# Kernel tuning notes

Hardware: AMD Instinct MI355X
Metric: run time of the kernel (lower is better)

The kernel has to match this reference:

```python
import jax, jax.numpy as jnp
import numpy as np

EMBED_DIM = 1024
K_DIM = 64
NUM_HEADS = 16


def setup_inputs() -> dict:
    key = jax.random.key(0)
    kx, kq, kk, kv, kw = jax.random.split(key, 5)
    x = jax.random.normal(kx, (4, 2048, EMBED_DIM), dtype=jnp.float32)
    # per-head weights stacked along a leading head axis (torch.randn init)
    wq = jax.random.normal(kq, (NUM_HEADS, EMBED_DIM, K_DIM), dtype=jnp.float32)
    wk = jax.random.normal(kk, (NUM_HEADS, EMBED_DIM, K_DIM), dtype=jnp.float32)
    wv = jax.random.normal(kv, (NUM_HEADS, EMBED_DIM, K_DIM), dtype=jnp.float32)
    w = jax.random.normal(kw, (NUM_HEADS * K_DIM, EMBED_DIM), dtype=jnp.float32)
    return {"x": x, "wq": wq, "wk": wk, "wv": wv, "w": w}


def reference(x, wq, wk, wv, w):
    # x: [B,S,D]; wq/wk/wv: [H,D,K]; w: [H*K, D]
    q = jnp.einsum('bsd,hdk->bhsk', x, wq)
    k = jnp.einsum('bsd,hdk->bhsk', x, wk)
    v = jnp.einsum('bsd,hdk->bhsk', x, wv)
    scale = 1.0 / jnp.sqrt(jnp.asarray(K_DIM, x.dtype))
    scores = jnp.einsum('bhsk,bhtk->bhst', q, k) * scale  # [B,H,S,S]
    attn = jax.nn.softmax(scores, axis=-1)
    ctx = jnp.einsum('bhst,bhtk->bhsk', attn, v)  # [B,H,S,K]
    B, H, S, K = ctx.shape
    # concat heads along last dim in head order (matches torch.cat of per-head outs)
    heads = jnp.transpose(ctx, (0, 2, 1, 3)).reshape(B, S, H * K)
    return jnp.matmul(heads, w)  # [B,S,D]
```

## Files before the change

kernel.cpp:

```cpp
#include <hip/hip_runtime.h>
#include <hip/hip_bf16.h>
#include <math.h>

#define EMBED 1024
#define KD 64
#define NH 16
#define SEQ 2048
#define BATCH 4
#define BH (BATCH * NH)
#define NTOK ((size_t)BH * SEQ * KD)

typedef float4 f4;
typedef unsigned short u16;
typedef __attribute__((ext_vector_type(8))) short v8s;
typedef __attribute__((ext_vector_type(4))) float v4f;

__device__ __forceinline__ u16 f2bf(float f) {
    unsigned u = __float_as_uint(f);
    unsigned r = (u + 0x7fffu + ((u >> 16) & 1u)) >> 16;
    return (u16)r;
}
__device__ __forceinline__ float bf2f(u16 h) {
    return __uint_as_float(((unsigned)h) << 16);
}

__device__ __forceinline__ void gload_lds16(const void* g, void* l) {
    __builtin_amdgcn_global_load_lds(
        (const __attribute__((address_space(1))) unsigned int*)g,
        (__attribute__((address_space(3))) unsigned int*)l, 16, 0, 0);
}

__device__ __forceinline__ float dpp_max16(float v) {
    float t;
    t = __uint_as_float(__builtin_amdgcn_update_dpp(0, __float_as_uint(v), 0xB1, 0xF, 0xF, true));
    v = fmaxf(v, t);
    t = __uint_as_float(__builtin_amdgcn_update_dpp(0, __float_as_uint(v), 0x4E, 0xF, 0xF, true));
    v = fmaxf(v, t);
    t = __uint_as_float(__builtin_amdgcn_update_dpp(0, __float_as_uint(v), 0x124, 0xF, 0xF, true));
    v = fmaxf(v, t);
    t = __uint_as_float(__builtin_amdgcn_update_dpp(0, __float_as_uint(v), 0x128, 0xF, 0xF, true));
    v = fmaxf(v, t);
    return v;
}

__global__ __launch_bounds__(256)
void convert_x_kernel(const float* __restrict__ x,
                      u16* __restrict__ xh, u16* __restrict__ xl)
{
    size_t i = ((size_t)blockIdx.x * 256 + threadIdx.x) * 4;
    f4 v = *(const f4*)(x + i);
    u16 h0 = f2bf(v.x), h1 = f2bf(v.y), h2 = f2bf(v.z), h3 = f2bf(v.w);
    u16 l0 = f2bf(v.x - bf2f(h0)), l1 = f2bf(v.y - bf2f(h1));
    u16 l2 = f2bf(v.z - bf2f(h2)), l3 = f2bf(v.w - bf2f(h3));
    uint2 H, L;
    H.x = (unsigned)h0 | ((unsigned)h1 << 16);
    H.y = (unsigned)h2 | ((unsigned)h3 << 16);
    L.x = (unsigned)l0 | ((unsigned)l1 << 16);
    L.y = (unsigned)l2 | ((unsigned)l3 << 16);
    *(uint2*)(xh + i) = H;
    *(uint2*)(xl + i) = L;
}

__global__ __launch_bounds__(256)
void convert_w_kernel(const float* __restrict__ wq, const float* __restrict__ wk,
                      const float* __restrict__ wv,
                      u16* __restrict__ Wth, u16* __restrict__ Wtl)
{
    int n = blockIdx.x;
    int mat = n >> 10, nin = n & 1023, h = nin >> 6, c = nin & 63;
    const float* __restrict__ ws = (mat == 0) ? wq : (mat == 1) ? wk : wv;
    float sc = (mat == 0) ? (0.125f * 1.4426950408889634f) : 1.0f;
    for (int d = threadIdx.x; d < EMBED; d += 256) {
        float f = ws[((size_t)h * EMBED + d) * KD + c] * sc;
        u16 hi = f2bf(f);
        u16 lo = f2bf(f - bf2f(hi));
        Wth[(size_t)n * EMBED + d] = hi;
        Wtl[(size_t)n * EMBED + d] = lo;
    }
}

__global__ __launch_bounds__(256)
void convert_ow_kernel(const float* __restrict__ w,
                       u16* __restrict__ OWth, u16* __restrict__ OWtl)
{
    int n = blockIdx.x;
    for (int k = threadIdx.x; k < EMBED; k += 256) {
        float f = w[(size_t)k * EMBED + n];
        u16 hi = f2bf(f);
        u16 lo = f2bf(f - bf2f(hi));
        OWth[(size_t)n * EMBED + k] = hi;
        OWtl[(size_t)n * EMBED + k] = lo;
    }
}

__global__ __launch_bounds__(256)
void qkv_mfma_kernel(const u16* __restrict__ xh, const u16* __restrict__ xl,
                     const u16* __restrict__ Wth, const u16* __restrict__ Wtl,
                     u16* __restrict__ Qhi, u16* __restrict__ Qlo,
                     u16* __restrict__ Khi, u16* __restrict__ Klo,
                     u16* __restrict__ Vt)
{
    __shared__ u16 sAh[128 * 64];
    __shared__ u16 sAl[128 * 64];
    __shared__ u16 sBh[128 * 64];
    __shared__ u16 sBl[128 * 64];
    const int tid = threadIdx.x;
    const int lane = tid & 63, wid = tid >> 6;
    const int lm = lane & 15, lq = lane >> 4;
    const int wm = wid & 1, wn = wid >> 1;
    const int m0 = blockIdx.y * 128;
    const int n0 = blockIdx.x * 128;
    const bool three = (n0 < 2048);

    v4f acc[4][4];
#pragma unroll
    for (int mt = 0; mt < 4; ++mt)
#pragma unroll
        for (int nt = 0; nt < 4; ++nt)
            acc[mt][nt] = (v4f){0.f, 0.f, 0.f, 0.f};

    const int srow = wid * 32 + (lane >> 3);
    const int sblk = (lane & 7) ^ (lane >> 3);

    for (int k0 = 0; k0 < EMBED; k0 += 64) {
        __syncthreads();
#pragma unroll
        for (int i = 0; i < 4; ++i) {
            int row = srow + i * 8;
            size_t gA = (((size_t)(m0 + row)) << 10) + k0 + sblk * 8;
            size_t gB = (((size_t)(n0 + row)) << 10) + k0 + sblk * 8;
            int lo = (wid * 32 + i * 8) * 128;
            gload_lds16((const char*)xh + gA * 2, (char*)sAh + lo);
            gload_lds16((const char*)Wth + gB * 2, (char*)sBh + lo);
            if (three) {
                gload_lds16((const char*)xl + gA * 2, (char*)sAl + lo);
                gload_lds16((const char*)Wtl + gB * 2, (char*)sBl + lo);
            }
        }
        asm volatile("s_waitcnt vmcnt(0)" ::: "memory");
        __syncthreads();

#pragma unroll
        for (int kks = 0; kks < 2; ++kks) {
            v8s ah[4], bh[4];
            const int ba = ((kks * 4 + lq) ^ (lm & 7)) * 8;
#pragma unroll
            for (int t = 0; t < 4; ++t) {
                int ra = wm * 64 + t * 16 + lm;
                int rb = wn * 64 + t * 16 + lm;
                ah[t] = *(const v8s*)&sAh[ra * 64 + ba];
                bh[t] = *(const v8s*)&sBh[rb * 64 + ba];
            }
            if (three) {
                v8s al[4], bl[4];
#pragma unroll
                for (int t = 0; t < 4; ++t) {
                    int ra = wm * 64 + t * 16 + lm;
                    int rb = wn * 64 + t * 16 + lm;
                    al[t] = *(const v8s*)&sAl[ra * 64 + ba];
                    bl[t] = *(const v8s*)&sBl[rb * 64 + ba];
                }
#pragma unroll
                for (int mt = 0; mt < 4; ++mt)
#pragma unroll
                    for (int nt = 0; nt < 4; ++nt) {
                        acc[mt][nt] = __builtin_amdgcn_mfma_f32_16x16x32_bf16(ah[mt], bh[nt], acc[mt][nt], 0, 0, 0);
                        acc[mt][nt] = __builtin_amdgcn_mfma_f32_16x16x32_bf16(ah[mt], bl[nt], acc[mt][nt], 0, 0, 0);
                        acc[mt][nt] = __builtin_amdgcn_mfma_f32_16x16x32_bf16(al[mt], bh[nt], acc[mt][nt], 0, 0, 0);
                    }
            } else {
#pragma unroll
                for (int mt = 0; mt < 4; ++mt)
#pragma unroll
                    for (int nt = 0; nt < 4; ++nt)
                        acc[mt][nt] = __builtin_amdgcn_mfma_f32_16x16x32_bf16(ah[mt], bh[nt], acc[mt][nt], 0, 0, 0);
            }
        }
    }

    const int mrow0 = m0 + wm * 64;
    const int ncol0 = n0 + wn * 64;
    if (!three) {
#pragma unroll
        for (int mt = 0; mt < 4; ++mt) {
            int sbase = mrow0 + mt * 16 + lq * 4;
            int bb = sbase >> 11, s = sbase & 2047;
#pragma unroll
            for (int nt = 0; nt < 4; ++nt) {
                int nin = (ncol0 + nt * 16 + lm) & 1023;
                int h = nin >> 6, cc = nin & 63;
                int bh_ = bb * NH + h;
                size_t a = ((size_t)bh_ * KD + cc) * SEQ
                         + (size_t)(((((s >> 3) ^ (cc & 7)) << 3)) | (s & 7));
                uint2 u;
                u.x = (unsigned)f2bf(acc[mt][nt][0]) | ((unsigned)f2bf(acc[mt][nt][1]) << 16);
                u.y = (unsigned)f2bf(acc[mt][nt][2]) | ((unsigned)f2bf(acc[mt][nt][3]) << 16);
                *(uint2*)(Vt + a) = u;
            }
        }
    } else {
        const bool isQ = (n0 < 1024);
#pragma unroll
        for (int mt = 0; mt < 4; ++mt) {
            int sbase = mrow0 + mt * 16 + lq * 4;
            int bb = sbase >> 11, sB = sbase & 2047;
#pragma unroll
            for (int nt = 0; nt < 4; ++nt) {
                int nin = (ncol0 + nt * 16 + lm) & 1023;
                int h = nin >> 6, cc = nin & 63;
                int bh_ = bb * NH + h;
#pragma unroll
                for (int r = 0; r < 4; ++r) {
                    int s = sB + r;
                    float f = acc[mt][nt][r];
                    u16 hi = f2bf(f);
                    u16 lo = f2bf(f - bf2f(hi));
                    if (isQ) {
                        size_t a = ((size_t)bh_ * SEQ + s) * KD + cc;
                        Qhi[a] = hi;
                        Qlo[a] = lo;
                    } else {
                        int ccp = ((((cc >> 3) ^ (s & 7)) << 3) | (cc & 7));
                        size_t a = ((size_t)bh_ * SEQ + s) * KD + ccp;
                        Khi[a] = hi;
                        Klo[a] = lo;
                    }
                }
            }
        }
    }
}

#define PSTRIDE 72

__global__ __launch_bounds__(256)
void attn_kernel(const u16* __restrict__ Qhi, const u16* __restrict__ Qlo,
                 const u16* __restrict__ Khi, const u16* __restrict__ Klo,
                 const u16* __restrict__ Vt,  u16* __restrict__ headsb)
{
    __shared__ u16 sKhi[64 * 64];
    __shared__ u16 sKlo[64 * 64];
    __shared__ u16 sVt[64 * 64];
    __shared__ u16 sPs[128 * PSTRIDE];

    const int tid = threadIdx.x;
    const int lane = tid & 63, wid = tid >> 6;
    const int lm = lane & 15, lq = lane >> 4;
    const int q0 = blockIdx.x * 128;
    const int bh = blockIdx.y;
    const int bb = bh >> 4, h = bh & 15;

    v8s qh[2][2], ql[2][2];
#pragma unroll
    for (int mt = 0; mt < 2; ++mt)
#pragma unroll
        for (int kk = 0; kk < 2; ++kk) {
            size_t g = ((size_t)bh * SEQ + q0 + wid * 32 + mt * 16 + lm) * KD
                     + kk * 32 + lq * 8;
            qh[mt][kk] = *(const v8s*)(Qhi + g);
            ql[mt][kk] = *(const v8s*)(Qlo + g);
        }

    v8s vones;
#pragma unroll
    for (int i = 0; i < 8; ++i) vones[i] = (short)0x3F80;

    v4f ctx[2][4], lcol[2];
    float mrun[2][4];
#pragma unroll
    for (int mt = 0; mt < 2; ++mt) {
        lcol[mt] = (v4f){0.f, 0.f, 0.f, 0.f};
#pragma unroll
        for (int r = 0; r < 4; ++r) mrun[mt][r] = -INFINITY;
#pragma unroll
        for (int nt = 0; nt < 4; ++nt)
            ctx[mt][nt] = (v4f){0.f, 0.f, 0.f, 0.f};
    }

    const size_t kbase = (size_t)bh * SEQ * KD;

    for (int t0 = 0; t0 < SEQ; t0 += 64) {
        __syncthreads();
        {
            const char* gk1 = (const char*)(Khi + kbase + (size_t)t0 * KD);
            const char* gk2 = (const char*)(Klo + kbase + (size_t)t0 * KD);
            int off = wid * 2048;
#pragma unroll
            for (int i = 0; i < 2; ++i) {
                int o = off + i * 1024;
                gload_lds16(gk1 + o + lane * 16, (char*)sKhi + o);
                gload_lds16(gk2 + o + lane * 16, (char*)sKlo + o);
            }
        }
#pragma unroll
        for (int i = 0; i < 2; ++i) {
            int row = wid * 16 + i * 8;
            const char* gv = (const char*)(Vt + ((size_t)bh * KD + row + (lane >> 3)) * SEQ + t0)
                           + (lane & 7) * 16;
            gload_lds16(gv, (char*)sVt + row * 128);
        }
        asm volatile("s_waitcnt vmcnt(0)" ::: "memory");
        __syncthreads();

        v4f sc[2][4];
#pragma unroll
        for (int mt = 0; mt < 2; ++mt)
#pragma unroll
            for (int nt = 0; nt < 4; ++nt)
                sc[mt][nt] = (v4f){0.f, 0.f, 0.f, 0.f};
#pragma unroll
        for (int kk = 0; kk < 2; ++kk) {
#pragma unroll
            for (int nt = 0; nt < 4; ++nt) {
                int key = nt * 16 + lm;
                int blk = (kk * 4 + lq) ^ (key & 7);
                v8s bh16 = *(const v8s*)&sKhi[key * 64 + blk * 8];
                v8s bl16 = *(const v8s*)&sKlo[key * 64 + blk * 8];
#pragma unroll
                for (int mt = 0; mt < 2; ++mt) {
                    sc[mt][nt] = __builtin_amdgcn_mfma_f32_16x16x32_bf16(qh[mt][kk], bh16, sc[mt][nt], 0, 0, 0);
                    sc[mt][nt] = __builtin_amdgcn_mfma_f32_16x16x32_bf16(qh[mt][kk], bl16, sc[mt][nt], 0, 0, 0);
                    sc[mt][nt] = __builtin_amdgcn_mfma_f32_16x16x32_bf16(ql[mt][kk], bh16, sc[mt][nt], 0, 0, 0);
                }
            }
        }

#pragma unroll
        for (int mt = 0; mt < 2; ++mt) {
#pragma unroll
            for (int r = 0; r < 4; ++r) {
                float v0 = sc[mt][0][r], v1 = sc[mt][1][r];
                float v2 = sc[mt][2][r], v3 = sc[mt][3][r];
                float mx = fmaxf(fmaxf(v0, v1), fmaxf(v2, v3));
                mx = dpp_max16(mx);
                float mold = mrun[mt][r];
                float mnew = fmaxf(mold, mx);
                float alpha = __builtin_amdgcn_exp2f(mold - mnew);
                mrun[mt][r] = mnew;
                float p0 = __builtin_amdgcn_exp2f(v0 - mnew);
                float p1 = __builtin_amdgcn_exp2f(v1 - mnew);
                float p2 = __builtin_amdgcn_exp2f(v2 - mnew);
                float p3 = __builtin_amdgcn_exp2f(v3 - mnew);
                lcol[mt][r] *= alpha;
#pragma unroll
                for (int nt = 0; nt < 4; ++nt)
                    ctx[mt][nt][r] *= alpha;
                int row = wid * 32 + mt * 16 + lq * 4 + r;
                sPs[row * PSTRIDE +  0 + lm] = f2bf(p0);
                sPs[row * PSTRIDE + 16 + lm] = f2bf(p1);
                sPs[row * PSTRIDE + 32 + lm] = f2bf(p2);
                sPs[row * PSTRIDE + 48 + lm] = f2bf(p3);
            }
        }

#pragma unroll
        for (int kk2 = 0; kk2 < 2; ++kk2) {
            v8s a[2];
#pragma unroll
            for (int mt = 0; mt < 2; ++mt)
                a[mt] = *(const v8s*)&sPs[(wid * 32 + mt * 16 + lm) * PSTRIDE + kk2 * 32 + lq * 8];
#pragma unroll
            for (int nt = 0; nt < 4; ++nt) {
                int hd = nt * 16 + lm;
                int blk = (kk2 * 4 + lq) ^ (hd & 7);
                v8s b = *(const v8s*)&sVt[hd * 64 + blk * 8];
#pragma unroll
                for (int mt = 0; mt < 2; ++mt)
                    ctx[mt][nt] = __builtin_amdgcn_mfma_f32_16x16x32_bf16(a[mt], b, ctx[mt][nt], 0, 0, 0);
            }
#pragma unroll
            for (int mt = 0; mt < 2; ++mt)
                lcol[mt] = __builtin_amdgcn_mfma_f32_16x16x32_bf16(a[mt], vones, lcol[mt], 0, 0, 0);
        }
    }

#pragma unroll
    for (int mt = 0; mt < 2; ++mt)
#pragma unroll
        for (int r = 0; r < 4; ++r) {
            int row = q0 + wid * 32 + mt * 16 + lq * 4 + r;
            float inv = 1.0f / lcol[mt][r];
            u16* dst = headsb + ((size_t)bb * SEQ + row) * EMBED + h * KD;
#pragma unroll
            for (int nt = 0; nt < 4; ++nt)
                dst[nt * 16 + lm] = f2bf(ctx[mt][nt][r] * inv);
        }
}

__global__ __launch_bounds__(256)
void out_mfma_kernel(const u16* __restrict__ headsb,
                     const u16* __restrict__ OWth, const u16* __restrict__ OWtl,
                     float* __restrict__ out)
{
    __shared__ u16 sA[128 * 64];
    __shared__ u16 sBh[128 * 64];
    __shared__ u16 sBl[128 * 64];
    const int tid = threadIdx.x;
    const int lane = tid & 63, wid = tid >> 6;
    const int lm = lane & 15, lq = lane >> 4;
    const int wm = wid & 1, wn = wid >> 1;
    const int m0 = blockIdx.y * 128;
    const int n0 = blockIdx.x * 128;

    v4f acc[4][4];
#pragma unroll
    for (int mt = 0; mt < 4; ++mt)
#pragma unroll
        for (int nt = 0; nt < 4; ++nt)
            acc[mt][nt] = (v4f){0.f, 0.f, 0.f, 0.f};

    const int srow = wid * 32 + (lane >> 3);
    const int sblk = (lane & 7) ^ (lane >> 3);

    for (int k0 = 0; k0 < EMBED; k0 += 64) {
        __syncthreads();
#pragma unroll
        for (int i = 0; i < 4; ++i) {
            int row = srow + i * 8;
            size_t gA = (((size_t)(m0 + row)) << 10) + k0 + sblk * 8;
            size_t gB = (((size_t)(n0 + row)) << 10) + k0 + sblk * 8;
            int lo = (wid * 32 + i * 8) * 128;
            gload_lds16((const char*)headsb + gA * 2, (char*)sA + lo);
            gload_lds16((const char*)OWth + gB * 2, (char*)sBh + lo);
            gload_lds16((const char*)OWtl + gB * 2, (char*)sBl + lo);
        }
        asm volatile("s_waitcnt vmcnt(0)" ::: "memory");
        __syncthreads();

#pragma unroll
        for (int kks = 0; kks < 2; ++kks) {
            const int ba = ((kks * 4 + lq) ^ (lm & 7)) * 8;
            v8s ah[4], bh[4], bl[4];
#pragma unroll
            for (int t = 0; t < 4; ++t) {
                int ra = wm * 64 + t * 16 + lm;
                int rb = wn * 64 + t * 16 + lm;
                ah[t] = *(const v8s*)&sA[ra * 64 + ba];
                bh[t] = *(const v8s*)&sBh[rb * 64 + ba];
                bl[t] = *(const v8s*)&sBl[rb * 64 + ba];
            }
#pragma unroll
            for (int mt = 0; mt < 4; ++mt)
#pragma unroll
                for (int nt = 0; nt < 4; ++nt) {
                    acc[mt][nt] = __builtin_amdgcn_mfma_f32_16x16x32_bf16(ah[mt], bh[nt], acc[mt][nt], 0, 0, 0);
                    acc[mt][nt] = __builtin_amdgcn_mfma_f32_16x16x32_bf16(ah[mt], bl[nt], acc[mt][nt], 0, 0, 0);
                }
        }
    }

    const int mrow0 = m0 + wm * 64;
    const int ncol0 = n0 + wn * 64;
#pragma unroll
    for (int mt = 0; mt < 4; ++mt) {
        int sbase = mrow0 + mt * 16 + lq * 4;
#pragma unroll
        for (int nt = 0; nt < 4; ++nt) {
            int n = ncol0 + nt * 16 + lm;
#pragma unroll
            for (int r = 0; r < 4; ++r)
                out[(size_t)(sbase + r) * EMBED + n] = acc[mt][nt][r];
        }
    }
}

extern "C" void kernel_launch(void* const* d_in, const int* in_sizes, int n_in,
                              void* d_out, int out_size, void* d_ws, size_t ws_size,
                              hipStream_t stream) {
    const float* x  = (const float*)d_in[0];
    const float* wq = (const float*)d_in[1];
    const float* wk = (const float*)d_in[2];
    const float* wv = (const float*)d_in[3];
    const float* w  = (const float*)d_in[4];
    float* out = (float*)d_out;

    u16* Qhi = (u16*)d_ws;
    u16* Qlo = Qhi + NTOK;
    u16* Khi = Qlo + NTOK;
    u16* Klo = Khi + NTOK;
    u16* Vt  = Klo + NTOK;
    u16* xh  = Vt + NTOK;
    u16* xl  = xh + NTOK;
    u16* Wth = xl + NTOK;
    u16* Wtl = Wth + (size_t)3072 * 1024;
    u16* OWth = Wtl + (size_t)3072 * 1024;
    u16* OWtl = OWth + (size_t)1024 * 1024;
    u16* headsb = xh;

    convert_x_kernel<<<8192, 256, 0, stream>>>(x, xh, xl);
    convert_w_kernel<<<3072, 256, 0, stream>>>(wq, wk, wv, Wth, Wtl);
    convert_ow_kernel<<<1024, 256, 0, stream>>>(w, OWth, OWtl);

    dim3 g1(24, 64);
    qkv_mfma_kernel<<<g1, 256, 0, stream>>>(xh, xl, Wth, Wtl, Qhi, Qlo, Khi, Klo, Vt);

    dim3 g2(SEQ / 128, BH);
    attn_kernel<<<g2, 256, 0, stream>>>(Qhi, Qlo, Khi, Klo, Vt, headsb);

    dim3 g3(8, 64);
    out_mfma_kernel<<<g3, 256, 0, stream>>>(headsb, OWth, OWtl, out);
}
```

Baseline: 500.6 us.

## Transpose score MFMA so softmax reductions stay in-lane; merge conversion kernels

The score MFMA operands are swapped to compute K·Q^T, so each lane holds a query column and the row max reduces mostly within registers plus two cross-row shuffles, replacing four DPP steps per row. P values are packed into bf16 pairs by truncation with perm and written as 8-byte stores. The rescale factor is redistributed to the accumulator layout with ds_bpermute. The three input-conversion kernels are merged into one launch to cut launch overhead. The truncating bf16 conversion of P slightly changes rounding compared with the old round-to-nearest path.

```diff
diff --git a/kernel.cpp b/kernel.cpp
--- a/kernel.cpp
+++ b/kernel.cpp
@@ -30,66 +30,49 @@
         (__attribute__((address_space(3))) unsigned int*)l, 16, 0, 0);
 }
 
-__device__ __forceinline__ float dpp_max16(float v) {
-    float t;
-    t = __uint_as_float(__builtin_amdgcn_update_dpp(0, __float_as_uint(v), 0xB1, 0xF, 0xF, true));
-    v = fmaxf(v, t);
-    t = __uint_as_float(__builtin_amdgcn_update_dpp(0, __float_as_uint(v), 0x4E, 0xF, 0xF, true));
-    v = fmaxf(v, t);
-    t = __uint_as_float(__builtin_amdgcn_update_dpp(0, __float_as_uint(v), 0x124, 0xF, 0xF, true));
-    v = fmaxf(v, t);
-    t = __uint_as_float(__builtin_amdgcn_update_dpp(0, __float_as_uint(v), 0x128, 0xF, 0xF, true));
-    v = fmaxf(v, t);
-    return v;
-}
-
 __global__ __launch_bounds__(256)
-void convert_x_kernel(const float* __restrict__ x,
-                      u16* __restrict__ xh, u16* __restrict__ xl)
+void convert_all_kernel(const float* __restrict__ x,
+                        const float* __restrict__ wq, const float* __restrict__ wk,
+                        const float* __restrict__ wv, const float* __restrict__ w,
+                        u16* __restrict__ xh, u16* __restrict__ xl,
+                        u16* __restrict__ Wth, u16* __restrict__ Wtl,
+                        u16* __restrict__ OWth, u16* __restrict__ OWtl)
 {
-    size_t i = ((size_t)blockIdx.x * 256 + threadIdx.x) * 4;
-    f4 v = *(const f4*)(x + i);
-    u16 h0 = f2bf(v.x), h1 = f2bf(v.y), h2 = f2bf(v.z), h3 = f2bf(v.w);
-    u16 l0 = f2bf(v.x - bf2f(h0)), l1 = f2bf(v.y - bf2f(h1));
-    u16 l2 = f2bf(v.z - bf2f(h2)), l3 = f2bf(v.w - bf2f(h3));
-    uint2 H, L;
-    H.x = (unsigned)h0 | ((unsigned)h1 << 16);
-    H.y = (unsigned)h2 | ((unsigned)h3 << 16);
-    L.x = (unsigned)l0 | ((unsigned)l1 << 16);
-    L.y = (unsigned)l2 | ((unsigned)l3 << 16);
-    *(uint2*)(xh + i) = H;
-    *(uint2*)(xl + i) = L;
-}
-
-__global__ __launch_bounds__(256)
-void convert_w_kernel(const float* __restrict__ wq, const float* __restrict__ wk,
-                      const float* __restrict__ wv,
-                      u16* __restrict__ Wth, u16* __restrict__ Wtl)
-{
-    int n = blockIdx.x;
-    int mat = n >> 10, nin = n & 1023, h = nin >> 6, c = nin & 63;
-    const float* __restrict__ ws = (mat == 0) ? wq : (mat == 1) ? wk : wv;
-    float sc = (mat == 0) ? (0.125f * 1.4426950408889634f) : 1.0f;
-    for (int d = threadIdx.x; d < EMBED; d += 256) {
-        float f = ws[((size_t)h * EMBED + d) * KD + c] * sc;
-        u16 hi = f2bf(f);
-        u16 lo = f2bf(f - bf2f(hi));
-        Wth[(size_t)n * EMBED + d] = hi;
-        Wtl[(size_t)n * EMBED + d] = lo;
-    }
-}
-
-__global__ __launch_bounds__(256)
-void convert_ow_kernel(const float* __restrict__ w,
-                       u16* __restrict__ OWth, u16* __restrict__ OWtl)
-{
-    int n = blockIdx.x;
-    for (int k = threadIdx.x; k < EMBED; k += 256) {
-        float f = w[(size_t)k * EMBED + n];
-        u16 hi = f2bf(f);
-        u16 lo = f2bf(f - bf2f(hi));
-        OWth[(size_t)n * EMBED + k] = hi;
-        OWtl[(size_t)n * EMBED + k] = lo;
+    int b = blockIdx.x;
+    if (b < 8192) {
+        size_t i = ((size_t)b * 256 + threadIdx.x) * 4;
+        f4 v = *(const f4*)(x + i);
+        u16 h0 = f2bf(v.x), h1 = f2bf(v.y), h2 = f2bf(v.z), h3 = f2bf(v.w);
+        u16 l0 = f2bf(v.x - bf2f(h0)), l1 = f2bf(v.y - bf2f(h1));
+        u16 l2 = f2bf(v.z - bf2f(h2)), l3 = f2bf(v.w - bf2f(h3));
+        uint2 H, L;
+        H.x = (unsigned)h0 | ((unsigned)h1 << 16);
+        H.y = (unsigned)h2 | ((unsigned)h3 << 16);
+        L.x = (unsigned)l0 | ((unsigned)l1 << 16);
+        L.y = (unsigned)l2 | ((unsigned)l3 << 16);
+        *(uint2*)(xh + i) = H;
+        *(uint2*)(xl + i) = L;
+    } else if (b < 8192 + 3072) {
+        int n = b - 8192;
+        int mat = n >> 10, nin = n & 1023, h = nin >> 6, c = nin & 63;
+        const float* __restrict__ ws = (mat == 0) ? wq : (mat == 1) ? wk : wv;
+        float sc = (mat == 0) ? (0.125f * 1.4426950408889634f) : 1.0f;
+        for (int d = threadIdx.x; d < EMBED; d += 256) {
+            float f = ws[((size_t)h * EMBED + d) * KD + c] * sc;
+            u16 hi = f2bf(f);
+            u16 lo = f2bf(f - bf2f(hi));
+            Wth[(size_t)n * EMBED + d] = hi;
+            Wtl[(size_t)n * EMBED + d] = lo;
+        }
+    } else {
+        int n = b - 11264;
+        for (int k = threadIdx.x; k < EMBED; k += 256) {
+            float f = w[(size_t)k * EMBED + n];
+            u16 hi = f2bf(f);
+            u16 lo = f2bf(f - bf2f(hi));
+            OWth[(size_t)n * EMBED + k] = hi;
+            OWtl[(size_t)n * EMBED + k] = lo;
+        }
     }
 }
 
@@ -252,29 +235,33 @@
 
     v8s qh[2][2], ql[2][2];
 #pragma unroll
-    for (int mt = 0; mt < 2; ++mt)
+    for (int qt = 0; qt < 2; ++qt)
 #pragma unroll
         for (int kk = 0; kk < 2; ++kk) {
-            size_t g = ((size_t)bh * SEQ + q0 + wid * 32 + mt * 16 + lm) * KD
+            size_t g = ((size_t)bh * SEQ + q0 + wid * 32 + qt * 16 + lm) * KD
                      + kk * 32 + lq * 8;
-            qh[mt][kk] = *(const v8s*)(Qhi + g);
-            ql[mt][kk] = *(const v8s*)(Qlo + g);
+            qh[qt][kk] = *(const v8s*)(Qhi + g);
+            ql[qt][kk] = *(const v8s*)(Qlo + g);
         }
 
     v8s vones;
 #pragma unroll
     for (int i = 0; i < 8; ++i) vones[i] = (short)0x3F80;
 
+    int bpaddr[4];
+#pragma unroll
+    for (int r = 0; r < 4; ++r)
+        bpaddr[r] = (((lane & 48) | (lq * 4 + r)) << 2);
+
     v4f ctx[2][4], lcol[2];
-    float mrun[2][4];
-#pragma unroll
-    for (int mt = 0; mt < 2; ++mt) {
-        lcol[mt] = (v4f){0.f, 0.f, 0.f, 0.f};
-#pragma unroll
-        for (int r = 0; r < 4; ++r) mrun[mt][r] = -INFINITY;
+    float mrun[2];
+#pragma unroll
+    for (int qt = 0; qt < 2; ++qt) {
+        lcol[qt] = (v4f){0.f, 0.f, 0.f, 0.f};
+        mrun[qt] = -INFINITY;
 #pragma unroll
         for (int nt = 0; nt < 4; ++nt)
-            ctx[mt][nt] = (v4f){0.f, 0.f, 0.f, 0.f};
+            ctx[qt][nt] = (v4f){0.f, 0.f, 0.f, 0.f};
     }
 
     const size_t kbase = (size_t)bh * SEQ * KD;
@@ -302,54 +289,67 @@
         asm volatile("s_waitcnt vmcnt(0)" ::: "memory");
         __syncthreads();
 
-        v4f sc[2][4];
-#pragma unroll
-        for (int mt = 0; mt < 2; ++mt)
-#pragma unroll
-            for (int nt = 0; nt < 4; ++nt)
-                sc[mt][nt] = (v4f){0.f, 0.f, 0.f, 0.f};
+        v4f sc[4][2];
+#pragma unroll
+        for (int kt = 0; kt < 4; ++kt)
+#pragma unroll
+            for (int qt = 0; qt < 2; ++qt)
+                sc[kt][qt] = (v4f){0.f, 0.f, 0.f, 0.f};
 #pragma unroll
         for (int kk = 0; kk < 2; ++kk) {
 #pragma unroll
-            for (int nt = 0; nt < 4; ++nt) {
-                int key = nt * 16 + lm;
+            for (int kt = 0; kt < 4; ++kt) {
+                int key = kt * 16 + lm;
                 int blk = (kk * 4 + lq) ^ (key & 7);
-                v8s bh16 = *(const v8s*)&sKhi[key * 64 + blk * 8];
-                v8s bl16 = *(const v8s*)&sKlo[key * 64 + blk * 8];
-#pragma unroll
-                for (int mt = 0; mt < 2; ++mt) {
-                    sc[mt][nt] = __builtin_amdgcn_mfma_f32_16x16x32_bf16(qh[mt][kk], bh16, sc[mt][nt], 0, 0, 0);
-                    sc[mt][nt] = __builtin_amdgcn_mfma_f32_16x16x32_bf16(qh[mt][kk], bl16, sc[mt][nt], 0, 0, 0);
-                    sc[mt][nt] = __builtin_amdgcn_mfma_f32_16x16x32_bf16(ql[mt][kk], bh16, sc[mt][nt], 0, 0, 0);
+                v8s kh16 = *(const v8s*)&sKhi[key * 64 + blk * 8];
+                v8s kl16 = *(const v8s*)&sKlo[key * 64 + blk * 8];
+#pragma unroll
+                for (int qt = 0; qt < 2; ++qt) {
+                    sc[kt][qt] = __builtin_amdgcn_mfma_f32_16x16x32_bf16(kh16, qh[qt][kk], sc[kt][qt], 0, 0, 0);
+                    sc[kt][qt] = __builtin_amdgcn_mfma_f32_16x16x32_bf16(kl16, qh[qt][kk], sc[kt][qt], 0, 0, 0);
+                    sc[kt][qt] = __builtin_amdgcn_mfma_f32_16x16x32_bf16(kh16, ql[qt][kk], sc[kt][qt], 0, 0, 0);
                 }
             }
         }
 
-#pragma unroll
-        for (int mt = 0; mt < 2; ++mt) {
+        float aq[2];
+#pragma unroll
+        for (int qt = 0; qt < 2; ++qt) {
+            float m0v = fmaxf(fmaxf(sc[0][qt][0], sc[0][qt][1]), fmaxf(sc[0][qt][2], sc[0][qt][3]));
+            float m1v = fmaxf(fmaxf(sc[1][qt][0], sc[1][qt][1]), fmaxf(sc[1][qt][2], sc[1][qt][3]));
+            float m2v = fmaxf(fmaxf(sc[2][qt][0], sc[2][qt][1]), fmaxf(sc[2][qt][2], sc[2][qt][3]));
+            float m3v = fmaxf(fmaxf(sc[3][qt][0], sc[3][qt][1]), fmaxf(sc[3][qt][2], sc[3][qt][3]));
+            float mx = fmaxf(fmaxf(m0v, m1v), fmaxf(m2v, m3v));
+            mx = fmaxf(mx, __shfl_xor(mx, 16));
+            mx = fmaxf(mx, __shfl_xor(mx, 32));
+            float mold = mrun[qt];
+            float mnew = fmaxf(mold, mx);
+            aq[qt] = __builtin_amdgcn_exp2f(mold - mnew);
+            mrun[qt] = mnew;
+            u16* pbase = &sPs[(wid * 32 + qt * 16 + lm) * PSTRIDE];
+#pragma unroll
+            for (int kt = 0; kt < 4; ++kt) {
+                unsigned u0 = __float_as_uint(__builtin_amdgcn_exp2f(sc[kt][qt][0] - mnew));
+                unsigned u1 = __float_as_uint(__builtin_amdgcn_exp2f(sc[kt][qt][1] - mnew));
+                unsigned u2 = __float_as_uint(__builtin_amdgcn_exp2f(sc[kt][qt][2] - mnew));
+                unsigned u3 = __float_as_uint(__builtin_amdgcn_exp2f(sc[kt][qt][3] - mnew));
+                uint2 pk;
+                pk.x = __builtin_amdgcn_perm(u1, u0, 0x07060302);
+                pk.y = __builtin_amdgcn_perm(u3, u2, 0x07060302);
+                *(uint2*)&pbase[kt * 16 + lq * 4] = pk;
+            }
+        }
+
+#pragma unroll
+        for (int qt = 0; qt < 2; ++qt) {
 #pragma unroll
             for (int r = 0; r < 4; ++r) {
-                float v0 = sc[mt][0][r], v1 = sc[mt][1][r];
-                float v2 = sc[mt][2][r], v3 = sc[mt][3][r];
-                float mx = fmaxf(fmaxf(v0, v1), fmaxf(v2, v3));
-                mx = dpp_max16(mx);
-                float mold = mrun[mt][r];
-                float mnew = fmaxf(mold, mx);
-                float alpha = __builtin_amdgcn_exp2f(mold - mnew);
-                mrun[mt][r] = mnew;
-                float p0 = __builtin_amdgcn_exp2f(v0 - mnew);
-                float p1 = __builtin_amdgcn_exp2f(v1 - mnew);
-                float p2 = __builtin_amdgcn_exp2f(v2 - mnew);
-                float p3 = __builtin_amdgcn_exp2f(v3 - mnew);
-                lcol[mt][r] *= alpha;
+                float ar = __uint_as_float(
+                    __builtin_amdgcn_ds_bpermute(bpaddr[r], __float_as_uint(aq[qt])));
+                lcol[qt][r] *= ar;
 #pragma unroll
                 for (int nt = 0; nt < 4; ++nt)
-                    ctx[mt][nt][r] *= alpha;
-                int row = wid * 32 + mt * 16 + lq * 4 + r;
-                sPs[row * PSTRIDE +  0 + lm] = f2bf(p0);
-                sPs[row * PSTRIDE + 16 + lm] = f2bf(p1);
-                sPs[row * PSTRIDE + 32 + lm] = f2bf(p2);
-                sPs[row * PSTRIDE + 48 + lm] = f2bf(p3);
+                    ctx[qt][nt][r] *= ar;
             }
         }
 
@@ -357,33 +357,33 @@
         for (int kk2 = 0; kk2 < 2; ++kk2) {
             v8s a[2];
 #pragma unroll
-            for (int mt = 0; mt < 2; ++mt)
-                a[mt] = *(const v8s*)&sPs[(wid * 32 + mt * 16 + lm) * PSTRIDE + kk2 * 32 + lq * 8];
+            for (int qt = 0; qt < 2; ++qt)
+                a[qt] = *(const v8s*)&sPs[(wid * 32 + qt * 16 + lm) * PSTRIDE + kk2 * 32 + lq * 8];
 #pragma unroll
             for (int nt = 0; nt < 4; ++nt) {
                 int hd = nt * 16 + lm;
                 int blk = (kk2 * 4 + lq) ^ (hd & 7);
                 v8s b = *(const v8s*)&sVt[hd * 64 + blk * 8];
 #pragma unroll
-                for (int mt = 0; mt < 2; ++mt)
-                    ctx[mt][nt] = __builtin_amdgcn_mfma_f32_16x16x32_bf16(a[mt], b, ctx[mt][nt], 0, 0, 0);
-            }
-#pragma unroll
-            for (int mt = 0; mt < 2; ++mt)
-                lcol[mt] = __builtin_amdgcn_mfma_f32_16x16x32_bf16(a[mt], vones, lcol[mt], 0, 0, 0);
-        }
-    }
-
-#pragma unroll
-    for (int mt = 0; mt < 2; ++mt)
+                for (int qt = 0; qt < 2; ++qt)
+                    ctx[qt][nt] = __builtin_amdgcn_mfma_f32_16x16x32_bf16(a[qt], b, ctx[qt][nt], 0, 0, 0);
+            }
+#pragma unroll
+            for (int qt = 0; qt < 2; ++qt)
+                lcol[qt] = __builtin_amdgcn_mfma_f32_16x16x32_bf16(a[qt], vones, lcol[qt], 0, 0, 0);
+        }
+    }
+
+#pragma unroll
+    for (int qt = 0; qt < 2; ++qt)
 #pragma unroll
         for (int r = 0; r < 4; ++r) {
-            int row = q0 + wid * 32 + mt * 16 + lq * 4 + r;
-            float inv = 1.0f / lcol[mt][r];
+            int row = q0 + wid * 32 + qt * 16 + lq * 4 + r;
+            float inv = 1.0f / lcol[qt][r];
             u16* dst = headsb + ((size_t)bb * SEQ + row) * EMBED + h * KD;
 #pragma unroll
             for (int nt = 0; nt < 4; ++nt)
-                dst[nt * 16 + lm] = f2bf(ctx[mt][nt][r] * inv);
+                dst[nt * 16 + lm] = f2bf(ctx[qt][nt][r] * inv);
         }
 }
 
@@ -487,9 +487,8 @@
     u16* OWtl = OWth + (size_t)1024 * 1024;
     u16* headsb = xh;
 
-    convert_x_kernel<<<8192, 256, 0, stream>>>(x, xh, xl);
-    convert_w_kernel<<<3072, 256, 0, stream>>>(wq, wk, wv, Wth, Wtl);
-    convert_ow_kernel<<<1024, 256, 0, stream>>>(w, OWth, OWtl);
+    convert_all_kernel<<<12288, 256, 0, stream>>>(x, wq, wk, wv, w,
+                                                  xh, xl, Wth, Wtl, OWth, OWtl);
 
     dim3 g1(24, 64);
     qkv_mfma_kernel<<<g1, 256, 0, stream>>>(xh, xl, Wth, Wtl, Qhi, Qlo, Khi, Klo, Vt);
```

Result: faster. 431.0 us (-13.9%).
